# Kernel optimization log

Hardware: AMD Instinct MI355X
Metric: run time of the kernel (lower is better)

## Reference

```python
import jax, jax.numpy as jnp
import numpy as np

D_MODEL = 1024
NUM_HEADS = 16
HEAD_DIM = D_MODEL // NUM_HEADS
SEQ_LEN = 2048
THETA = 10000.0


def setup_inputs() -> dict:
    key = jax.random.key(0)
    ks = jax.random.split(key, 9)
    s = 1.0 / np.sqrt(D_MODEL)
    inp = {
        "x": jax.random.normal(ks[0], (2, SEQ_LEN, D_MODEL), dtype=jnp.float32),
        "Wq": jax.random.uniform(ks[1], (D_MODEL, D_MODEL), jnp.float32, -s, s),
        "bq": jax.random.uniform(ks[2], (D_MODEL,), jnp.float32, -s, s),
        "Wk": jax.random.uniform(ks[3], (D_MODEL, D_MODEL), jnp.float32, -s, s),
        "bk": jax.random.uniform(ks[4], (D_MODEL,), jnp.float32, -s, s),
        "Wv": jax.random.uniform(ks[5], (D_MODEL, D_MODEL), jnp.float32, -s, s),
        "bv": jax.random.uniform(ks[6], (D_MODEL,), jnp.float32, -s, s),
        "Wo": jax.random.uniform(ks[7], (D_MODEL, D_MODEL), jnp.float32, -s, s),
        "bo": jax.random.uniform(ks[8], (D_MODEL,), jnp.float32, -s, s),
    }
    return inp


def _rope_cos_sin(seq_len, dim, theta):
    inv_freq = 1.0 / theta ** (jnp.arange(0, dim, 2, dtype=jnp.float32) / dim)  # [dim/2]
    t = jnp.arange(seq_len, dtype=jnp.float32)
    freqs = jnp.outer(t, inv_freq)  # [S, dim/2]
    return jnp.cos(freqs), jnp.sin(freqs)


def _apply_rope(x, cos, sin):
    # x: [B, H, S, head_dim]; interleaved complex pairs (even, odd)
    x2 = x.reshape(*x.shape[:-1], -1, 2)  # [B,H,S,hd/2,2]
    xe, xo = x2[..., 0], x2[..., 1]
    c = cos[None, None, :, :]
    s = sin[None, None, :, :]
    oe = xe * c - xo * s
    oo = xe * s + xo * c
    return jnp.stack([oe, oo], axis=-1).reshape(x.shape)


def reference(x, Wq, bq, Wk, bk, Wv, bv, Wo, bo):
    B, S, D = x.shape
    H, hd = NUM_HEADS, HEAD_DIM
    q = x @ Wq.T + bq
    k = x @ Wk.T + bk
    v = x @ Wv.T + bv
    # [B, H, S, hd]
    q = q.reshape(B, S, H, hd).transpose(0, 2, 1, 3)
    k = k.reshape(B, S, H, hd).transpose(0, 2, 1, 3)
    v = v.reshape(B, S, H, hd).transpose(0, 2, 1, 3)
    cos, sin = _rope_cos_sin(S, hd, THETA)
    q = _apply_rope(q, cos, sin)
    k = _apply_rope(k, cos, sin)
    scores = jnp.einsum("bhqd,bhkd->bhqk", q, k) / jnp.sqrt(jnp.float32(hd))
    causal = jnp.triu(jnp.ones((S, S), dtype=bool), k=1)
    scores = jnp.where(causal[None, None, :, :], -jnp.inf, scores)
    attn = jax.nn.softmax(scores, axis=-1)
    out = jnp.einsum("bhqk,bhkd->bhqd", attn, v)
    out = out.transpose(0, 2, 1, 3).reshape(B, S, D)
    return out @ Wo.T + bo
```

## Files before the change

kernel.cpp:

```cpp
#include <hip/hip_runtime.h>
#include <hip/hip_bf16.h>

#define S_LEN 2048
#define DM 1024
#define NH 16
#define HD 64
#define M_ROWS 4096
#define LOG2E 1.4426950408889634f
#define MASKVAL -1.0e4f
#define QSCALE 0.18033688011112042f

typedef __attribute__((ext_vector_type(8))) short short8;
typedef __attribute__((ext_vector_type(4))) float f32x4;
typedef __attribute__((ext_vector_type(16))) float f32x16;

__device__ inline ushort f2b(float f) {
  union { float f; unsigned u; } v; v.f = f;
  unsigned r = v.u + 0x7fffu + ((v.u >> 16) & 1u);
  return (ushort)(r >> 16);
}

__device__ inline float b2f(ushort u) {
  union { unsigned u; float f; } v; v.u = ((unsigned)u) << 16; return v.f;
}

__device__ inline unsigned pk_bf16(float a, float b) {
  __hip_bfloat162 h = __float22bfloat162_rn(make_float2(a, b));
  union { __hip_bfloat162 h; unsigned u; } v; v.h = h;
  return v.u;
}

__device__ inline float fexp2(float x) { return __builtin_amdgcn_exp2f(x); }

__device__ inline void gl_lds16(const void* g, void* l) {
  __builtin_amdgcn_global_load_lds(
      (const __attribute__((address_space(1))) void*)g,
      (__attribute__((address_space(3))) void*)l, 16, 0, 0);
}

__global__ __launch_bounds__(256) void cast_rope_kernel(
    const float* __restrict__ x, const float* __restrict__ Wq, const float* __restrict__ Wk,
    const float* __restrict__ Wv, const float* __restrict__ Wo,
    ushort* __restrict__ xb, ushort* __restrict__ Wqb, ushort* __restrict__ Wkb,
    ushort* __restrict__ Wvb, ushort* __restrict__ Wob,
    float* __restrict__ ropeC, float* __restrict__ ropeS) {
  const int bid = blockIdx.x;
  if (bid >= 8192) {
    int idx = (bid - 8192) * 256 + threadIdx.x;
    int s = idx >> 5, i = idx & 31;
    float inv = exp2f(-(float)i * (13.287712379549449f / 32.0f));
    float a = (float)s * inv;
    ropeC[idx] = cosf(a);
    ropeS[idx] = sinf(a);
    return;
  }
  int i = bid * 256 + threadIdx.x;
  int r = i >> 18, off = i & 0x3FFFF;
  const float4* s;
  uint2* d;
  switch (r) {
    case 0: case 1: case 2: case 3: s = (const float4*)x + i;  d = (uint2*)xb + i;  break;
    case 4: s = (const float4*)Wq + off; d = (uint2*)Wqb + off; break;
    case 5: s = (const float4*)Wk + off; d = (uint2*)Wkb + off; break;
    case 6: s = (const float4*)Wv + off; d = (uint2*)Wvb + off; break;
    default: s = (const float4*)Wo + off; d = (uint2*)Wob + off; break;
  }
  float4 v = *s;
  uint2 o;
  o.x = pk_bf16(v.x, v.y);
  o.y = pk_bf16(v.z, v.w);
  *d = o;
}

__global__ __launch_bounds__(256) void gemm_qkv_kernel(const ushort* __restrict__ xb,
    const ushort* __restrict__ Wqb, const ushort* __restrict__ Wkb, const ushort* __restrict__ Wvb,
    const float* __restrict__ bq, const float* __restrict__ bk, const float* __restrict__ bv,
    const float* __restrict__ ropeC, const float* __restrict__ ropeS,
    ushort* __restrict__ qb, ushort* __restrict__ kb, ushort* __restrict__ vT) {
  __shared__ ushort lds[17408];
  ushort* As = lds;
  ushort* Bs = lds + 8192;
  const int z = blockIdx.z;
  const ushort* W = (z == 0) ? Wqb : ((z == 1) ? Wkb : Wvb);
  const float* bias = (z == 0) ? bq : ((z == 1) ? bk : bv);
  const int m0 = blockIdx.x * 128, n0 = blockIdx.y * 128;
  const int t = threadIdx.x, lane = t & 63, wave = t >> 6;
  const int wr = (wave >> 1) * 64, wc = (wave & 1) * 64;
  const int lr = lane & 15, lg = lane >> 4;

  const int slot0 = wave * 128 + lane, slot1 = slot0 + 64;
  const int row0 = slot0 >> 2, g0 = (slot0 & 3) ^ (row0 & 3);
  const int row1 = slot1 >> 2, g1 = (slot1 & 3) ^ (row1 & 3);
  const ushort* Ap0 = &xb[(size_t)(m0 + row0) * DM + g0 * 8];
  const ushort* Ap1 = &xb[(size_t)(m0 + row1) * DM + g1 * 8];
  const ushort* Wp0 = &W[(size_t)(n0 + row0) * DM + g0 * 8];
  const ushort* Wp1 = &W[(size_t)(n0 + row1) * DM + g1 * 8];

  f32x4 acc[4][4];
#pragma unroll
  for (int a = 0; a < 4; a++)
#pragma unroll
    for (int b = 0; b < 4; b++) acc[a][b] = (f32x4){0.f, 0.f, 0.f, 0.f};

  gl_lds16(Ap0, &As[slot0 * 8]);
  gl_lds16(Ap1, &As[slot1 * 8]);
  gl_lds16(Wp0, &Bs[slot0 * 8]);
  gl_lds16(Wp1, &Bs[slot1 * 8]);
  __syncthreads();

  int buf = 0;
  for (int i = 0; i < 32; i++) {
    if (i + 1 < 32) {
      const int k0 = (i + 1) * 32;
      const int bo = (buf ^ 1) * 4096;
      gl_lds16(Ap0 + k0, &As[bo + slot0 * 8]);
      gl_lds16(Ap1 + k0, &As[bo + slot1 * 8]);
      gl_lds16(Wp0 + k0, &Bs[bo + slot0 * 8]);
      gl_lds16(Wp1 + k0, &Bs[bo + slot1 * 8]);
    }
    const int fb = buf * 4096;
    short8 af[4], bf[4];
#pragma unroll
    for (int mt = 0; mt < 4; mt++) {
      const int row = wr + mt * 16 + lr;
      af[mt] = *(const short8*)&As[fb + (row * 4 + (lg ^ (row & 3))) * 8];
    }
#pragma unroll
    for (int nt = 0; nt < 4; nt++) {
      const int row = wc + nt * 16 + lr;
      bf[nt] = *(const short8*)&Bs[fb + (row * 4 + (lg ^ (row & 3))) * 8];
    }
#pragma unroll
    for (int mt = 0; mt < 4; mt++)
#pragma unroll
      for (int nt = 0; nt < 4; nt++)
        acc[mt][nt] = __builtin_amdgcn_mfma_f32_16x16x32_bf16(af[mt], bf[nt], acc[mt][nt], 0, 0, 0);
    __syncthreads();
    buf ^= 1;
  }

#pragma unroll
  for (int mt = 0; mt < 4; mt++) {
#pragma unroll
    for (int nt = 0; nt < 4; nt++) {
      const int nloc = wc + nt * 16 + lr;
      const float bn = bias[n0 + nloc];
#pragma unroll
      for (int r = 0; r < 4; r++) {
        const int mloc = wr + mt * 16 + lg * 4 + r;
        const ushort v = f2b(acc[mt][nt][r] + bn);
        if (z < 2) lds[mloc * 136 + nloc] = v;
        else       lds[nloc * 136 + mloc] = v;
      }
    }
  }
  __syncthreads();

  const int b = m0 >> 11;
  if (z < 2) {
    ushort* dst = (z == 0) ? qb : kb;
    const float qscale = (z == 0) ? QSCALE : 1.0f;
#pragma unroll
    for (int c = 0; c < 8; c++) {
      const int sloc = c * 16 + (t >> 4);
      const int nloc = (t & 15) * 8;
      short8 val = *(const short8*)&lds[sloc * 136 + nloc];
      const int s = (m0 + sloc) & (S_LEN - 1);
      const int h = (n0 + nloc) >> 6;
      const int d0 = nloc & 63;
      const float4 cv = *(const float4*)&ropeC[s * 32 + d0 / 2];
      const float4 sv = *(const float4*)&ropeS[s * 32 + d0 / 2];
      uint4 o;
      {
        float e = b2f((ushort)val[0]), od = b2f((ushort)val[1]);
        o.x = pk_bf16((e * cv.x - od * sv.x) * qscale, (e * sv.x + od * cv.x) * qscale);
      }
      {
        float e = b2f((ushort)val[2]), od = b2f((ushort)val[3]);
        o.y = pk_bf16((e * cv.y - od * sv.y) * qscale, (e * sv.y + od * cv.y) * qscale);
      }
      {
        float e = b2f((ushort)val[4]), od = b2f((ushort)val[5]);
        o.z = pk_bf16((e * cv.z - od * sv.z) * qscale, (e * sv.z + od * cv.z) * qscale);
      }
      {
        float e = b2f((ushort)val[6]), od = b2f((ushort)val[7]);
        o.w = pk_bf16((e * cv.w - od * sv.w) * qscale, (e * sv.w + od * cv.w) * qscale);
      }
      *(uint4*)&dst[(((size_t)b * NH + h) * S_LEN + s) * HD + d0] = o;
    }
  } else {
    const int sbase = m0 & (S_LEN - 1);
#pragma unroll
    for (int c = 0; c < 8; c++) {
      const int nloc = c * 16 + (t >> 4);
      const int s0 = (t & 15) * 8;
      short8 val = *(const short8*)&lds[nloc * 136 + s0];
      const int h = (n0 + nloc) >> 6;
      const int d = nloc & 63;
      *(short8*)&vT[(((size_t)b * NH + h) * HD + d) * S_LEN + sbase + s0] = val;
    }
  }
}

__global__ __launch_bounds__(256) void flash_kernel(const ushort* __restrict__ qb,
                                                    const ushort* __restrict__ kb,
                                                    const ushort* __restrict__ vT,
                                                    ushort* __restrict__ Oh,
                                                    float* __restrict__ lsum) {
  __shared__ ushort Ks[2][4096];
  __shared__ ushort VTs[2][4096];
  const int t = threadIdx.x, lane = t & 63, wave = t >> 6;
  const int q31 = lane & 31, h = lane >> 5;
  const int bh = blockIdx.y;
  const int cid = blockIdx.x;
  const int g = (cid >= 24) ? 3 : (cid >= 12) ? 2 : (cid >= 4) ? 1 : 0;
  const int nc = g + 1;
  const int o = cid - 4 * ((g * (g + 1)) >> 1);
  const int qi = o / nc;
  const int c = o - qi * nc;
  const int qt = g * 4 + qi;
  const int q0 = qt * 128;
  const int ntiles = 2 * qt + 2;
  const int kstart = c * 8;
  const int kend = min(kstart + 8, ntiles);
  const int pidx = bh * 40 + cid;

  const ushort* kbh = kb + (size_t)bh * S_LEN * HD;
  const ushort* vbh = vT + (size_t)bh * HD * S_LEN;

  const int qrow = q0 + wave * 32 + q31;
  const ushort* qptr = qb + ((size_t)bh * S_LEN + qrow) * HD + h * 8;
  short8 qf[4];
#pragma unroll
  for (int s = 0; s < 4; s++) qf[s] = *(const short8*)(qptr + s * 16);

  const int slot0 = wave * 128 + lane, slot1 = slot0 + 64;
  const int row0 = slot0 >> 3, g0 = (slot0 & 7) ^ (row0 & 7);
  const int row1 = slot1 >> 3, g1 = (slot1 & 7) ^ (row1 & 7);
  const int lo0 = wave * 128 * 8, lo1 = lo0 + 64 * 8;

  int foff[4][2];
#pragma unroll
  for (int s = 0; s < 4; s++)
#pragma unroll
    for (int st = 0; st < 2; st++) {
      const int row = st * 32 + q31;
      foff[s][st] = (row * 8 + ((2 * s + h) ^ (row & 7))) * 8;
    }

  {
    const int k00 = kstart * 64;
    gl_lds16(kbh + (size_t)(k00 + row0) * HD + g0 * 8, &Ks[0][lo0]);
    gl_lds16(kbh + (size_t)(k00 + row1) * HD + g1 * 8, &Ks[0][lo1]);
    gl_lds16(vbh + (size_t)row0 * S_LEN + k00 + g0 * 8, &VTs[0][lo0]);
    gl_lds16(vbh + (size_t)row1 * S_LEN + k00 + g1 * 8, &VTs[0][lo1]);
  }
  __syncthreads();

  f32x16 O[2];
#pragma unroll
  for (int st = 0; st < 2; st++)
#pragma unroll
    for (int r = 0; r < 16; r++) O[st][r] = 0.f;
  float lacc = 0.f;
  int cur = 0;

  for (int kt = kstart; kt < kend; kt++) {
    if (kt + 1 < kend) {
      const int k0n = (kt + 1) * 64;
      gl_lds16(kbh + (size_t)(k0n + row0) * HD + g0 * 8, &Ks[cur ^ 1][lo0]);
      gl_lds16(kbh + (size_t)(k0n + row1) * HD + g1 * 8, &Ks[cur ^ 1][lo1]);
      gl_lds16(vbh + (size_t)row0 * S_LEN + k0n + g0 * 8, &VTs[cur ^ 1][lo0]);
      gl_lds16(vbh + (size_t)row1 * S_LEN + k0n + g1 * 8, &VTs[cur ^ 1][lo1]);
    }
    const ushort* Kb = Ks[cur];
    const ushort* Vb = VTs[cur];

    f32x16 sc[2];
#pragma unroll
    for (int st = 0; st < 2; st++)
#pragma unroll
      for (int r = 0; r < 16; r++) sc[st][r] = 0.f;
    __builtin_amdgcn_s_setprio(1);
#pragma unroll
    for (int s = 0; s < 4; s++) {
#pragma unroll
      for (int st = 0; st < 2; st++) {
        const short8 kf = *(const short8*)&Kb[foff[s][st]];
        sc[st] = __builtin_amdgcn_mfma_f32_32x32x16_bf16(kf, qf[s], sc[st], 0, 0, 0);
      }
    }
    __builtin_amdgcn_s_setprio(0);
    if (kt * 64 + 63 > q0 + wave * 32) {
#pragma unroll
      for (int st = 0; st < 2; st++)
#pragma unroll
        for (int r = 0; r < 16; r++) {
          const int kcol = kt * 64 + st * 32 + (r & 3) + 8 * (r >> 2) + 4 * h;
          if (kcol > qrow) sc[st][r] = MASKVAL;
        }
    }
    float lp0 = 0.f, lp1 = 0.f, lp2 = 0.f, lp3 = 0.f;
#pragma unroll
    for (int st = 0; st < 2; st++)
#pragma unroll
      for (int r = 0; r < 16; r += 4) {
        const float p0 = fexp2(sc[st][r + 0]);
        const float p1 = fexp2(sc[st][r + 1]);
        const float p2 = fexp2(sc[st][r + 2]);
        const float p3 = fexp2(sc[st][r + 3]);
        sc[st][r + 0] = p0;
        sc[st][r + 1] = p1;
        sc[st][r + 2] = p2;
        sc[st][r + 3] = p3;
        lp0 += p0; lp1 += p1; lp2 += p2; lp3 += p3;
      }
    lacc += (lp0 + lp1) + (lp2 + lp3);

    unsigned pp[8][2];
#pragma unroll
    for (int st = 0; st < 2; st++)
#pragma unroll
      for (int rg = 0; rg < 4; rg++) {
        pp[st * 4 + rg][0] = pk_bf16(sc[st][4 * rg + 0], sc[st][4 * rg + 1]);
        pp[st * 4 + rg][1] = pk_bf16(sc[st][4 * rg + 2], sc[st][4 * rg + 3]);
      }
    __builtin_amdgcn_s_setprio(1);
#pragma unroll
    for (int s = 0; s < 4; s++) {
      unsigned d0 = pp[2 * s][0], e0 = pp[2 * s + 1][0];
      unsigned d1 = pp[2 * s][1], e1 = pp[2 * s + 1][1];
      asm("v_permlane32_swap_b32 %0, %1" : "+v"(d0), "+v"(e0));
      asm("v_permlane32_swap_b32 %0, %1" : "+v"(d1), "+v"(e1));
      union { unsigned u[4]; short8 v; } pf;
      pf.u[0] = d0;
      pf.u[1] = d1;
      pf.u[2] = e0;
      pf.u[3] = e1;
#pragma unroll
      for (int st = 0; st < 2; st++) {
        const short8 vf = *(const short8*)&Vb[foff[s][st]];
        O[st] = __builtin_amdgcn_mfma_f32_32x32x16_bf16(vf, pf.v, O[st], 0, 0, 0);
      }
    }
    __builtin_amdgcn_s_setprio(0);
    __syncthreads();
    cur ^= 1;
  }

  lacc += __shfl_xor(lacc, 32);

  ushort* obase = Oh + ((size_t)pidx * 128 + wave * 32 + q31) * HD;
#pragma unroll
  for (int st = 0; st < 2; st++)
#pragma unroll
    for (int rg = 0; rg < 4; rg++) {
      const int d0 = st * 32 + 8 * rg + 4 * h;
      uint2 w;
      w.x = pk_bf16(O[st][4 * rg + 0], O[st][4 * rg + 1]);
      w.y = pk_bf16(O[st][4 * rg + 2], O[st][4 * rg + 3]);
      *(uint2*)&obase[d0] = w;
    }
  if (h == 0) lsum[(size_t)pidx * 128 + wave * 32 + q31] = lacc;
}

__global__ __launch_bounds__(256) void combine_kernel(const ushort* __restrict__ Oh,
                                                      const float* __restrict__ lsum,
                                                      ushort* __restrict__ attn) {
  const int tid = blockIdx.x * 256 + threadIdx.x;
  const int d8 = tid & 7;
  const int q = (tid >> 3) & (S_LEN - 1);
  const int bh = tid >> 14;
  const int qt = q >> 7, row = q & 127;
  const int g = qt >> 2, nc = g + 1;
  const int base = 4 * ((g * (g + 1)) >> 1) + (qt & 3) * nc;
  const int p0 = bh * 40 + base;

  float l = 0.f;
  float acc[8];
#pragma unroll
  for (int j = 0; j < 8; j++) acc[j] = 0.f;
  for (int c = 0; c < nc; c++) {
    const size_t rowidx = (size_t)(p0 + c) * 128 + row;
    l += lsum[rowidx];
    const uint4 a = *(const uint4*)&Oh[rowidx * HD + d8 * 8];
    const unsigned au[4] = {a.x, a.y, a.z, a.w};
#pragma unroll
    for (int j = 0; j < 4; j++) {
      acc[2 * j] += b2f((ushort)(au[j] & 0xffff));
      acc[2 * j + 1] += b2f((ushort)(au[j] >> 16));
    }
  }
  const float inv = 1.f / l;
  uint4 o;
  unsigned* op = (unsigned*)&o;
#pragma unroll
  for (int j = 0; j < 4; j++) op[j] = pk_bf16(acc[2 * j] * inv, acc[2 * j + 1] * inv);
  const int b = bh >> 4, hh = bh & 15;
  *(uint4*)&attn[((size_t)b * S_LEN + q) * DM + hh * HD + d8 * 8] = o;
}

__global__ __launch_bounds__(256) void gemm_out_kernel(const ushort* __restrict__ attn,
                                                       const ushort* __restrict__ Wob,
                                                       const float* __restrict__ bo,
                                                       float* __restrict__ out) {
  __shared__ ushort As[2][4096];
  __shared__ ushort Bs[2][2048];
  const int m0 = blockIdx.x * 128, n0 = blockIdx.y * 64;
  const int t = threadIdx.x, lane = t & 63, wave = t >> 6;
  const int wm = (wave >> 1) * 64, wn = (wave & 1) * 32;
  const int lr = lane & 15, lg = lane >> 4;
  const int slotA0 = wave * 128 + lane, slotA1 = slotA0 + 64;
  const int rowA0 = slotA0 >> 2, gA0 = (slotA0 & 3) ^ (rowA0 & 3);
  const int rowA1 = slotA1 >> 2, gA1 = (slotA1 & 3) ^ (rowA1 & 3);
  const int slotB = wave * 64 + lane;
  const int rowB = slotB >> 2, gB = (slotB & 3) ^ (rowB & 3);
  const ushort* Ap0 = &attn[(size_t)(m0 + rowA0) * DM + gA0 * 8];
  const ushort* Ap1 = &attn[(size_t)(m0 + rowA1) * DM + gA1 * 8];
  const ushort* Wp  = &Wob[(size_t)(n0 + rowB) * DM + gB * 8];

  f32x4 acc[4][2];
#pragma unroll
  for (int a = 0; a < 4; a++)
#pragma unroll
    for (int b = 0; b < 2; b++) acc[a][b] = (f32x4){0.f, 0.f, 0.f, 0.f};

  gl_lds16(Ap0, &As[0][slotA0 * 8]);
  gl_lds16(Ap1, &As[0][slotA1 * 8]);
  gl_lds16(Wp, &Bs[0][slotB * 8]);
  __syncthreads();

  int buf = 0;
  for (int i = 0; i < 32; i++) {
    if (i + 1 < 32) {
      const int k0 = (i + 1) * 32;
      gl_lds16(Ap0 + k0, &As[buf ^ 1][slotA0 * 8]);
      gl_lds16(Ap1 + k0, &As[buf ^ 1][slotA1 * 8]);
      gl_lds16(Wp + k0, &Bs[buf ^ 1][slotB * 8]);
    }
    short8 af[4], bf[2];
#pragma unroll
    for (int mt = 0; mt < 4; mt++) {
      const int row = wm + mt * 16 + lr;
      af[mt] = *(const short8*)&As[buf][(row * 4 + (lg ^ (row & 3))) * 8];
    }
#pragma unroll
    for (int nt = 0; nt < 2; nt++) {
      const int row = wn + nt * 16 + lr;
      bf[nt] = *(const short8*)&Bs[buf][(row * 4 + (lg ^ (row & 3))) * 8];
    }
#pragma unroll
    for (int mt = 0; mt < 4; mt++)
#pragma unroll
      for (int nt = 0; nt < 2; nt++)
        acc[mt][nt] = __builtin_amdgcn_mfma_f32_16x16x32_bf16(af[mt], bf[nt], acc[mt][nt], 0, 0, 0);
    __syncthreads();
    buf ^= 1;
  }

#pragma unroll
  for (int mt = 0; mt < 4; mt++) {
#pragma unroll
    for (int nt = 0; nt < 2; nt++) {
      const int n = n0 + wn + nt * 16 + lr;
      const float bn = bo[n];
#pragma unroll
      for (int r = 0; r < 4; r++) {
        const int m = m0 + wm + mt * 16 + lg * 4 + r;
        out[(size_t)m * DM + n] = acc[mt][nt][r] + bn;
      }
    }
  }
}

extern "C" void kernel_launch(void* const* d_in, const int* in_sizes, int n_in,
                              void* d_out, int out_size, void* d_ws, size_t ws_size,
                              hipStream_t stream) {
  const float* x  = (const float*)d_in[0];
  const float* Wq = (const float*)d_in[1];
  const float* bq = (const float*)d_in[2];
  const float* Wk = (const float*)d_in[3];
  const float* bk = (const float*)d_in[4];
  const float* Wv = (const float*)d_in[5];
  const float* bv = (const float*)d_in[6];
  const float* Wo = (const float*)d_in[7];
  const float* bo = (const float*)d_in[8];
  float* out = (float*)d_out;

  char* ws = (char*)d_ws;
  size_t off = 0;
  auto alloc = [&](size_t bytes) { char* p = ws + off; off += (bytes + 255) & ~255ull; return p; };
  ushort* xb   = (ushort*)alloc((size_t)M_ROWS * DM * 2);
  ushort* Wqb  = (ushort*)alloc((size_t)DM * DM * 2);
  ushort* Wkb  = (ushort*)alloc((size_t)DM * DM * 2);
  ushort* Wvb  = (ushort*)alloc((size_t)DM * DM * 2);
  ushort* Wob  = (ushort*)alloc((size_t)DM * DM * 2);
  ushort* qb   = (ushort*)alloc((size_t)M_ROWS * DM * 2);
  ushort* kb   = (ushort*)alloc((size_t)M_ROWS * DM * 2);
  ushort* vTb  = (ushort*)alloc((size_t)M_ROWS * DM * 2);
  ushort* attn = (ushort*)alloc((size_t)M_ROWS * DM * 2);
  ushort* Ohb  = (ushort*)alloc((size_t)1280 * 128 * HD * 2);
  float* lsb   = (float*)alloc((size_t)1280 * 128 * 4);
  float* ropeC = (float*)alloc((size_t)S_LEN * 32 * 4);
  float* ropeS = (float*)alloc((size_t)S_LEN * 32 * 4);
  (void)ws_size; (void)in_sizes; (void)n_in; (void)out_size;

  cast_rope_kernel<<<8448, 256, 0, stream>>>(x, Wq, Wk, Wv, Wo, xb, Wqb, Wkb, Wvb, Wob,
                                             ropeC, ropeS);
  gemm_qkv_kernel<<<dim3(M_ROWS / 128, DM / 128, 3), 256, 0, stream>>>(
      xb, Wqb, Wkb, Wvb, bq, bk, bv, ropeC, ropeS, qb, kb, vTb);
  flash_kernel<<<dim3(40, 32), 256, 0, stream>>>(qb, kb, vTb, Ohb, lsb);
  combine_kernel<<<2048, 256, 0, stream>>>(Ohb, lsb, attn);
  gemm_out_kernel<<<dim3(M_ROWS / 128, DM / 64), 256, 0, stream>>>(attn, Wob, bo, out);
}
```

Baseline: 192.7 us.

## Triple-buffer K/V tiles in flash kernel with manual vmcnt-gated barriers

Replaces the double-buffered K/V LDS staging with a three-deep ring buffer and prefetches two tiles ahead. The full __syncthreads is replaced by an explicit s_waitcnt vmcnt plus s_barrier, so the wait covers only the tile about to be used while the next one stays in flight. Also starts the score MFMA chain from a zero accumulator and keeps the row sums as packed float2 values. The aim is to hide global-to-LDS latency better, at the cost of more LDS per block (48 KB instead of 32 KB), which may lower occupancy.

Measured after the change: 193.7 us. No clear change (+0.5%).

```diff
diff --git a/kernel.cpp b/kernel.cpp
--- a/kernel.cpp
+++ b/kernel.cpp
@@ -11,6 +11,7 @@
 #define QSCALE 0.18033688011112042f
 
 typedef __attribute__((ext_vector_type(8))) short short8;
+typedef __attribute__((ext_vector_type(2))) float f32x2;
 typedef __attribute__((ext_vector_type(4))) float f32x4;
 typedef __attribute__((ext_vector_type(16))) float f32x16;
 
@@ -208,8 +209,7 @@
                                                     const ushort* __restrict__ vT,
                                                     ushort* __restrict__ Oh,
                                                     float* __restrict__ lsum) {
-  __shared__ ushort Ks[2][4096];
-  __shared__ ushort VTs[2][4096];
+  __shared__ ushort lds[24576];
   const int t = threadIdx.x, lane = t & 63, wave = t >> 6;
   const int q31 = lane & 31, h = lane >> 5;
   const int bh = blockIdx.y;
@@ -249,83 +249,93 @@
       foff[s][st] = (row * 8 + ((2 * s + h) ^ (row & 7))) * 8;
     }
 
-  {
-    const int k00 = kstart * 64;
-    gl_lds16(kbh + (size_t)(k00 + row0) * HD + g0 * 8, &Ks[0][lo0]);
-    gl_lds16(kbh + (size_t)(k00 + row1) * HD + g1 * 8, &Ks[0][lo1]);
-    gl_lds16(vbh + (size_t)row0 * S_LEN + k00 + g0 * 8, &VTs[0][lo0]);
-    gl_lds16(vbh + (size_t)row1 * S_LEN + k00 + g1 * 8, &VTs[0][lo1]);
-  }
-  __syncthreads();
+  const ushort* kp0 = kbh + (size_t)(kstart * 64 + row0) * HD + g0 * 8;
+  const ushort* kp1 = kbh + (size_t)(kstart * 64 + row1) * HD + g1 * 8;
+  const ushort* vp0 = vbh + (size_t)row0 * S_LEN + kstart * 64 + g0 * 8;
+  const ushort* vp1 = vbh + (size_t)row1 * S_LEN + kstart * 64 + g1 * 8;
+  gl_lds16(kp0, &lds[lo0]);
+  gl_lds16(kp1, &lds[lo1]);
+  gl_lds16(vp0, &lds[12288 + lo0]);
+  gl_lds16(vp1, &lds[12288 + lo1]);
+  kp0 += 64 * HD; kp1 += 64 * HD; vp0 += 64; vp1 += 64;
+  gl_lds16(kp0, &lds[4096 + lo0]);
+  gl_lds16(kp1, &lds[4096 + lo1]);
+  gl_lds16(vp0, &lds[16384 + lo0]);
+  gl_lds16(vp1, &lds[16384 + lo1]);
+  kp0 += 64 * HD; kp1 += 64 * HD; vp0 += 64; vp1 += 64;
 
   f32x16 O[2];
 #pragma unroll
   for (int st = 0; st < 2; st++)
 #pragma unroll
     for (int r = 0; r < 16; r++) O[st][r] = 0.f;
-  float lacc = 0.f;
+
+  f32x16 zc;
+#pragma unroll
+  for (int r = 0; r < 16; r++) zc[r] = 0.f;
+
+  f32x2 lpA = (f32x2){0.f, 0.f}, lpB = (f32x2){0.f, 0.f};
+
+  asm volatile("s_waitcnt vmcnt(4)" ::: "memory");
+  __builtin_amdgcn_s_barrier();
+  __builtin_amdgcn_sched_barrier(0);
+
   int cur = 0;
-
-  for (int kt = kstart; kt < kend; kt++) {
-    if (kt + 1 < kend) {
-      const int k0n = (kt + 1) * 64;
-      gl_lds16(kbh + (size_t)(k0n + row0) * HD + g0 * 8, &Ks[cur ^ 1][lo0]);
-      gl_lds16(kbh + (size_t)(k0n + row1) * HD + g1 * 8, &Ks[cur ^ 1][lo1]);
-      gl_lds16(vbh + (size_t)row0 * S_LEN + k0n + g0 * 8, &VTs[cur ^ 1][lo0]);
-      gl_lds16(vbh + (size_t)row1 * S_LEN + k0n + g1 * 8, &VTs[cur ^ 1][lo1]);
-    }
-    const ushort* Kb = Ks[cur];
-    const ushort* Vb = VTs[cur];
-
-    f32x16 sc[2];
-#pragma unroll
-    for (int st = 0; st < 2; st++)
-#pragma unroll
-      for (int r = 0; r < 16; r++) sc[st][r] = 0.f;
+  for (int kt = kstart; kt < kend; ++kt) {
+    const bool pref = (kt + 2 < kend);
+    if (pref) {
+      const int nb = (cur >= 1) ? cur - 1 : 2;
+      const int ko = nb * 4096, vo = 12288 + nb * 4096;
+      gl_lds16(kp0, &lds[ko + lo0]);
+      gl_lds16(kp1, &lds[ko + lo1]);
+      gl_lds16(vp0, &lds[vo + lo0]);
+      gl_lds16(vp1, &lds[vo + lo1]);
+      kp0 += 64 * HD; kp1 += 64 * HD; vp0 += 64; vp1 += 64;
+    }
+    const ushort* Kb = &lds[cur * 4096];
+    const ushort* Vb = &lds[12288 + cur * 4096];
+
+    f32x16 sc0, sc1;
     __builtin_amdgcn_s_setprio(1);
-#pragma unroll
-    for (int s = 0; s < 4; s++) {
-#pragma unroll
-      for (int st = 0; st < 2; st++) {
-        const short8 kf = *(const short8*)&Kb[foff[s][st]];
-        sc[st] = __builtin_amdgcn_mfma_f32_32x32x16_bf16(kf, qf[s], sc[st], 0, 0, 0);
-      }
+    sc0 = __builtin_amdgcn_mfma_f32_32x32x16_bf16(
+        *(const short8*)&Kb[foff[0][0]], qf[0], zc, 0, 0, 0);
+    sc1 = __builtin_amdgcn_mfma_f32_32x32x16_bf16(
+        *(const short8*)&Kb[foff[0][1]], qf[0], zc, 0, 0, 0);
+#pragma unroll
+    for (int s = 1; s < 4; s++) {
+      sc0 = __builtin_amdgcn_mfma_f32_32x32x16_bf16(
+          *(const short8*)&Kb[foff[s][0]], qf[s], sc0, 0, 0, 0);
+      sc1 = __builtin_amdgcn_mfma_f32_32x32x16_bf16(
+          *(const short8*)&Kb[foff[s][1]], qf[s], sc1, 0, 0, 0);
     }
     __builtin_amdgcn_s_setprio(0);
+
     if (kt * 64 + 63 > q0 + wave * 32) {
 #pragma unroll
-      for (int st = 0; st < 2; st++)
-#pragma unroll
-        for (int r = 0; r < 16; r++) {
-          const int kcol = kt * 64 + st * 32 + (r & 3) + 8 * (r >> 2) + 4 * h;
-          if (kcol > qrow) sc[st][r] = MASKVAL;
-        }
-    }
-    float lp0 = 0.f, lp1 = 0.f, lp2 = 0.f, lp3 = 0.f;
-#pragma unroll
-    for (int st = 0; st < 2; st++)
-#pragma unroll
-      for (int r = 0; r < 16; r += 4) {
-        const float p0 = fexp2(sc[st][r + 0]);
-        const float p1 = fexp2(sc[st][r + 1]);
-        const float p2 = fexp2(sc[st][r + 2]);
-        const float p3 = fexp2(sc[st][r + 3]);
-        sc[st][r + 0] = p0;
-        sc[st][r + 1] = p1;
-        sc[st][r + 2] = p2;
-        sc[st][r + 3] = p3;
-        lp0 += p0; lp1 += p1; lp2 += p2; lp3 += p3;
-      }
-    lacc += (lp0 + lp1) + (lp2 + lp3);
+      for (int r = 0; r < 16; r++) {
+        const int kc0 = kt * 64 + (r & 3) + 8 * (r >> 2) + 4 * h;
+        if (kc0 > qrow) sc0[r] = MASKVAL;
+        if (kc0 + 32 > qrow) sc1[r] = MASKVAL;
+      }
+    }
+#pragma unroll
+    for (int r = 0; r < 16; r += 2) {
+      const float a0 = fexp2(sc0[r]), a1 = fexp2(sc0[r + 1]);
+      const float b0 = fexp2(sc1[r]), b1 = fexp2(sc1[r + 1]);
+      sc0[r] = a0; sc0[r + 1] = a1;
+      sc1[r] = b0; sc1[r + 1] = b1;
+      lpA += (f32x2){a0, a1};
+      lpB += (f32x2){b0, b1};
+    }
 
     unsigned pp[8][2];
 #pragma unroll
-    for (int st = 0; st < 2; st++)
-#pragma unroll
-      for (int rg = 0; rg < 4; rg++) {
-        pp[st * 4 + rg][0] = pk_bf16(sc[st][4 * rg + 0], sc[st][4 * rg + 1]);
-        pp[st * 4 + rg][1] = pk_bf16(sc[st][4 * rg + 2], sc[st][4 * rg + 3]);
-      }
+    for (int rg = 0; rg < 4; rg++) {
+      pp[rg][0] = pk_bf16(sc0[4 * rg + 0], sc0[4 * rg + 1]);
+      pp[rg][1] = pk_bf16(sc0[4 * rg + 2], sc0[4 * rg + 3]);
+      pp[4 + rg][0] = pk_bf16(sc1[4 * rg + 0], sc1[4 * rg + 1]);
+      pp[4 + rg][1] = pk_bf16(sc1[4 * rg + 2], sc1[4 * rg + 3]);
+    }
     __builtin_amdgcn_s_setprio(1);
 #pragma unroll
     for (int s = 0; s < 4; s++) {
@@ -338,17 +348,23 @@
       pf.u[1] = d1;
       pf.u[2] = e0;
       pf.u[3] = e1;
-#pragma unroll
-      for (int st = 0; st < 2; st++) {
-        const short8 vf = *(const short8*)&Vb[foff[s][st]];
-        O[st] = __builtin_amdgcn_mfma_f32_32x32x16_bf16(vf, pf.v, O[st], 0, 0, 0);
-      }
+      O[0] = __builtin_amdgcn_mfma_f32_32x32x16_bf16(
+          *(const short8*)&Vb[foff[s][0]], pf.v, O[0], 0, 0, 0);
+      O[1] = __builtin_amdgcn_mfma_f32_32x32x16_bf16(
+          *(const short8*)&Vb[foff[s][1]], pf.v, O[1], 0, 0, 0);
     }
     __builtin_amdgcn_s_setprio(0);
-    __syncthreads();
-    cur ^= 1;
-  }
-
+
+    if (kt + 1 < kend) {
+      if (pref) asm volatile("s_waitcnt vmcnt(4)" ::: "memory");
+      else      asm volatile("s_waitcnt vmcnt(0)" ::: "memory");
+      __builtin_amdgcn_s_barrier();
+      __builtin_amdgcn_sched_barrier(0);
+    }
+    cur = (cur >= 2) ? 0 : cur + 1;
+  }
+
+  float lacc = (lpA[0] + lpA[1]) + (lpB[0] + lpB[1]);
   lacc += __shfl_xor(lacc, 32);
 
   ushort* obase = Oh + ((size_t)pidx * 128 + wave * 32 + q31) * HD;
```
